# Kernel optimization log

Measured on AMD Instinct MI355X. Metric: run time of the kernel, lower is better.

Reference implementation:

```python
import jax, jax.numpy as jnp
import numpy as np

PROJ = 8192     # projDim
THRESH = 1e-8   # numerical-stability epsilon for signed sqrt
L2_EPS = 1e-12  # eps of torch F.normalize


def setup_inputs() -> dict:
    key = jax.random.key(0)
    k1, k2, k3, k4, k5 = jax.random.split(key, 5)
    B, C, H, W = 16, 512, 14, 14
    x = jax.random.normal(k1, (B, C, H, W), dtype=jnp.float32)
    h1 = jax.random.randint(k2, (C,), 0, PROJ, dtype=jnp.int32)
    h2 = jax.random.randint(k3, (C,), 0, PROJ, dtype=jnp.int32)
    s1 = (2 * jax.random.randint(k4, (C,), 0, 2) - 1).astype(jnp.float32)
    s2 = (2 * jax.random.randint(k5, (C,), 0, 2) - 1).astype(jnp.float32)
    return {"x": x, "s1": s1, "s2": s2, "h1": h1, "h2": h2}


def reference(x, s1, s2, h1, h2):
    # x: [B, C, H, W]; h*: [C] hash buckets in [0, PROJ); s*: [C] signs (+-1)
    B, C, H, W = x.shape
    x_flat = jnp.transpose(x, (0, 2, 3, 1)).reshape(-1, C)  # [N, C], N = B*H*W

    def count_sketch(s, h):
        # Equivalent to x_flat @ M with M[c, h[c]] = s[c]: scatter-add of
        # sign-weighted channels into PROJ bins.  -> [N, PROJ]
        return jax.ops.segment_sum((x_flat * s).T, h, num_segments=PROJ).T

    fft1 = jnp.fft.fft(count_sketch(s1, h1), axis=-1)
    fft2 = jnp.fft.fft(count_sketch(s2, h2), axis=-1)
    conv = jnp.fft.ifft(fft1 * fft2, axis=-1).real       # [N, PROJ]
    y = conv.reshape(B, H, W, PROJ).sum(axis=(1, 2))      # sum pool -> [B, PROJ]
    y = jnp.sign(y) * jnp.sqrt(jnp.abs(y) + THRESH)       # signed sqrt
    norm = jnp.linalg.norm(y, axis=1, keepdims=True)
    return y / jnp.maximum(norm, L2_EPS)                  # l2 normalize (dim=1)
```

## Files before the change

kernel.cpp:

```cpp
#include <hip/hip_runtime.h>
#include <math.h>

#define PROJ 8192
#define NB   16
#define NC   512
#define HW   196
#define NKC  7
#define LST  40

typedef __attribute__((ext_vector_type(8))) short bf16x8;
typedef __attribute__((ext_vector_type(4))) short short4v;
typedef __attribute__((ext_vector_type(4))) float f32x4;

__device__ __forceinline__ unsigned bf16_rne(float f) {
    unsigned u = __builtin_bit_cast(unsigned, f);
    return (u + 0x7fffu + ((u >> 16) & 1u)) >> 16;
}

__global__ __launch_bounds__(256)
void cbp_gram_mfma(const float* __restrict__ x,
                   const float* __restrict__ s1,
                   const float* __restrict__ s2,
                   const int*   __restrict__ h1,
                   const int*   __restrict__ h2,
                   float* __restrict__ ws) {
    __shared__ float sk[PROJ];
    __shared__ short Ah[128 * LST];
    __shared__ short Al[128 * LST];
    __shared__ short Bh[128 * LST];
    __shared__ short Bl[128 * LST];
    __shared__ int   lh1[128], lh2[128];
    __shared__ float ls1[128], ls2[128];

    const int tid  = threadIdx.x;
    const int blk  = blockIdx.x;
    const int b    = blk >> 4;
    const int I    = (blk >> 2) & 3;
    const int J    = blk & 3;
    const int c1base = I * 128;
    const int c2base = J * 128;

    const int lane = tid & 63;
    const int wave = tid >> 6;
    const int quad = lane >> 4;
    const int l15  = lane & 15;
    const int wr   = (wave >> 1) * 64;
    const int wc   = (wave & 1) * 64;

    for (int i = tid; i < PROJ; i += 256) sk[i] = 0.f;
    if (tid < 128) {
        lh1[tid] = h1[c1base + tid]; ls1[tid] = s1[c1base + tid];
        lh2[tid] = h2[c2base + tid]; ls2[tid] = s2[c2base + tid];
    }

    const float* xa = x + ((size_t)b * NC + c1base) * HW;
    const float* xb = x + ((size_t)b * NC + c2base) * HW;

    f32x4 acc[4][4];
#pragma unroll
    for (int i = 0; i < 4; ++i)
#pragma unroll
        for (int j = 0; j < 4; ++j)
            acc[i][j] = (f32x4){0.f, 0.f, 0.f, 0.f};

    for (int kc = 0; kc < NKC; ++kc) {
        const int k0 = kc * 32;
        __syncthreads();
#pragma unroll
        for (int it = 0; it < 4; ++it) {
            const int s  = tid + 256 * it;
            const int r  = s >> 3;
            const int q  = s & 7;
            const int kk = k0 + 4 * q;
            float4 va = {0.f, 0.f, 0.f, 0.f}, vb = {0.f, 0.f, 0.f, 0.f};
            if (kk + 3 < HW) {
                va = *(const float4*)&xa[r * HW + kk];
                vb = *(const float4*)&xb[r * HW + kk];
            }
            short4v ah, al, bh, bl;
            const float fa[4] = {va.x, va.y, va.z, va.w};
            const float fb[4] = {vb.x, vb.y, vb.z, vb.w};
#pragma unroll
            for (int c = 0; c < 4; ++c) {
                const unsigned ha_ = bf16_rne(fa[c]);
                ah[c] = (short)ha_;
                al[c] = (short)bf16_rne(fa[c] - __builtin_bit_cast(float, ha_ << 16));
                const unsigned hb_ = bf16_rne(fb[c]);
                bh[c] = (short)hb_;
                bl[c] = (short)bf16_rne(fb[c] - __builtin_bit_cast(float, hb_ << 16));
            }
            *(short4v*)&Ah[r * LST + 4 * q] = ah;
            *(short4v*)&Al[r * LST + 4 * q] = al;
            *(short4v*)&Bh[r * LST + 4 * q] = bh;
            *(short4v*)&Bl[r * LST + 4 * q] = bl;
        }
        __syncthreads();

        bf16x8 ahf[4], alf[4], bhf[4], blf[4];
#pragma unroll
        for (int i = 0; i < 4; ++i) {
            const int ra = wr + i * 16 + l15;
            const int rb = wc + i * 16 + l15;
            ahf[i] = *(const bf16x8*)&Ah[ra * LST + quad * 8];
            alf[i] = *(const bf16x8*)&Al[ra * LST + quad * 8];
            bhf[i] = *(const bf16x8*)&Bh[rb * LST + quad * 8];
            blf[i] = *(const bf16x8*)&Bl[rb * LST + quad * 8];
        }
#pragma unroll
        for (int i = 0; i < 4; ++i)
#pragma unroll
            for (int j = 0; j < 4; ++j) {
                acc[i][j] = __builtin_amdgcn_mfma_f32_16x16x32_bf16(ahf[i], bhf[j], acc[i][j], 0, 0, 0);
                acc[i][j] = __builtin_amdgcn_mfma_f32_16x16x32_bf16(ahf[i], blf[j], acc[i][j], 0, 0, 0);
                acc[i][j] = __builtin_amdgcn_mfma_f32_16x16x32_bf16(alf[i], bhf[j], acc[i][j], 0, 0, 0);
            }
    }
    __syncthreads();

#pragma unroll
    for (int i = 0; i < 4; ++i) {
        const int lr0 = wr + i * 16 + quad * 4;
#pragma unroll
        for (int j = 0; j < 4; ++j) {
            const int lc   = wc + j * 16 + l15;
            const int h2v  = lh2[lc];
            const float s2v = ls2[lc];
#pragma unroll
            for (int rg = 0; rg < 4; ++rg) {
                const int lr  = lr0 + rg;
                const int bin = (lh1[lr] + h2v) & (PROJ - 1);
                atomicAdd(&sk[bin], ls1[lr] * s2v * acc[i][j][rg]);
            }
        }
    }
    __syncthreads();

    float4* dst = (float4*)(ws + (size_t)blk * PROJ);
    const float4* src = (const float4*)sk;
    for (int i = tid; i < PROJ / 4; i += 256) dst[i] = src[i];
}

__global__ __launch_bounds__(256)
void cbp_reduce(const float* __restrict__ ws, float* __restrict__ y,
                float* __restrict__ ssqp) {
    const int blk = blockIdx.x;
    const int b   = blk >> 5;
    const int seg = blk & 31;
    const int tid = threadIdx.x;
    const int bin = seg * 256 + tid;

    const float* base = ws + (size_t)b * 16 * PROJ + bin;
    float s = 0.f;
#pragma unroll
    for (int p = 0; p < 16; ++p) s += base[(size_t)p * PROJ];

    const float m = sqrtf(fabsf(s) + 1e-8f);
    const float o = (s > 0.f) ? m : (s < 0.f ? -m : 0.f);
    y[b * PROJ + bin] = o;

    __shared__ float red[256];
    red[tid] = o * o;
    __syncthreads();
#pragma unroll
    for (int st = 128; st >= 1; st >>= 1) {
        if (tid < st) red[tid] += red[tid + st];
        __syncthreads();
    }
    if (tid == 0) ssqp[blk] = red[0];
}

__global__ __launch_bounds__(256)
void cbp_normalize(float* __restrict__ y, const float* __restrict__ ssqp) {
    const int b   = blockIdx.x >> 1;
    const int off = (blockIdx.x & 1) * 4096;
    const int tid = threadIdx.x;
    float ssq = 0.f;
#pragma unroll
    for (int i = 0; i < 32; ++i) ssq += ssqp[b * 32 + i];
    const float inv = 1.0f / fmaxf(sqrtf(ssq), 1e-12f);

    float4* row = (float4*)&y[(size_t)b * PROJ + off];
#pragma unroll
    for (int j = 0; j < 4; ++j) {
        float4 v = row[j * 256 + tid];
        v.x *= inv; v.y *= inv; v.z *= inv; v.w *= inv;
        row[j * 256 + tid] = v;
    }
}

extern "C" void kernel_launch(void* const* d_in, const int* in_sizes, int n_in,
                              void* d_out, int out_size, void* d_ws, size_t ws_size,
                              hipStream_t stream) {
    const float* x  = (const float*)d_in[0];
    const float* s1 = (const float*)d_in[1];
    const float* s2 = (const float*)d_in[2];
    const int*   h1 = (const int*)d_in[3];
    const int*   h2 = (const int*)d_in[4];
    float* y    = (float*)d_out;
    float* ws   = (float*)d_ws;
    float* ssqp = ws + (size_t)256 * PROJ;

    hipLaunchKernelGGL(cbp_gram_mfma, dim3(NB * 16), dim3(256), 0, stream,
                       x, s1, s2, h1, h2, ws);
    hipLaunchKernelGGL(cbp_reduce, dim3(512), dim3(256), 0, stream, ws, y, ssqp);
    hipLaunchKernelGGL(cbp_normalize, dim3(32), dim3(256), 0, stream, y, ssqp);
}
```

Baseline: 111.2 us.

## Double workgroup size, prefetch next K chunk into registers, fold signs into inputs

The Gram MFMA kernel moves to 512-thread workgroups, so each of 8 waves owns a 32x64 sub-tile instead of 64x64. The next K-chunk of x is now loaded from global memory into registers while the current chunk is converted and computed, to hide load latency behind the bf16 split and MFMA work. The hash signs are multiplied into the inputs before the hi/lo bf16 split, which takes the per-element sign multiplies out of the atomic scatter. The block-to-batch mapping is also remapped to interleave batches, and the reduce kernel's workspace indexing is updated to match. In exchange, each thread holds more registers for the prefetch, and per-wave tiles are smaller, which lowers B-fragment reuse per wave.

After: 104.2 us. -6.3%, faster.

```diff
diff --git a/kernel.cpp b/kernel.cpp
--- a/kernel.cpp
+++ b/kernel.cpp
@@ -17,7 +17,7 @@
     return (u + 0x7fffu + ((u >> 16) & 1u)) >> 16;
 }
 
-__global__ __launch_bounds__(256)
+__global__ __launch_bounds__(512, 2)
 void cbp_gram_mfma(const float* __restrict__ x,
                    const float* __restrict__ s1,
                    const float* __restrict__ s2,
@@ -30,13 +30,13 @@
     __shared__ short Bh[128 * LST];
     __shared__ short Bl[128 * LST];
     __shared__ int   lh1[128], lh2[128];
-    __shared__ float ls1[128], ls2[128];
-
-    const int tid  = threadIdx.x;
-    const int blk  = blockIdx.x;
-    const int b    = blk >> 4;
-    const int I    = (blk >> 2) & 3;
-    const int J    = blk & 3;
+    __shared__ float lsA[128], lsB[128];
+
+    const int tid = threadIdx.x;
+    const int blk = blockIdx.x;
+    const int b    = 2 * (blk & 7) + (blk >> 7);
+    const int tile = (blk >> 3) & 15;
+    const int I = tile >> 2, J = tile & 3;
     const int c1base = I * 128;
     const int c2base = J * 128;
 
@@ -44,42 +44,48 @@
     const int wave = tid >> 6;
     const int quad = lane >> 4;
     const int l15  = lane & 15;
-    const int wr   = (wave >> 1) * 64;
+    const int wr   = (wave >> 1) * 32;
     const int wc   = (wave & 1) * 64;
 
-    for (int i = tid; i < PROJ; i += 256) sk[i] = 0.f;
+    for (int i = tid; i < PROJ; i += 512) sk[i] = 0.f;
     if (tid < 128) {
-        lh1[tid] = h1[c1base + tid]; ls1[tid] = s1[c1base + tid];
-        lh2[tid] = h2[c2base + tid]; ls2[tid] = s2[c2base + tid];
+        lh1[tid] = h1[c1base + tid];  lsA[tid] = s1[c1base + tid];
+        lh2[tid] = h2[c2base + tid];  lsB[tid] = s2[c2base + tid];
     }
 
     const float* xa = x + ((size_t)b * NC + c1base) * HW;
     const float* xb = x + ((size_t)b * NC + c2base) * HW;
 
-    f32x4 acc[4][4];
-#pragma unroll
-    for (int i = 0; i < 4; ++i)
-#pragma unroll
-        for (int j = 0; j < 4; ++j)
-            acc[i][j] = (f32x4){0.f, 0.f, 0.f, 0.f};
+    f32x4 acc[2][4];
+#pragma unroll
+    for (int i = 0; i < 2; ++i)
+#pragma unroll
+        for (int j = 0; j < 4; ++j) acc[i][j] = (f32x4){0.f, 0.f, 0.f, 0.f};
+
+    const int sr0 = tid >> 3;
+    const int sq  = tid & 7;
+
+    float4 pa[2], pb[2];
+    {
+        const int kk = 4 * sq;
+        const bool ok = (kk + 3 < HW);
+#pragma unroll
+        for (int h = 0; h < 2; ++h) {
+            const int r = sr0 + 64 * h;
+            pa[h] = ok ? *(const float4*)&xa[r * HW + kk] : (float4){0.f,0.f,0.f,0.f};
+            pb[h] = ok ? *(const float4*)&xb[r * HW + kk] : (float4){0.f,0.f,0.f,0.f};
+        }
+    }
 
     for (int kc = 0; kc < NKC; ++kc) {
-        const int k0 = kc * 32;
         __syncthreads();
 #pragma unroll
-        for (int it = 0; it < 4; ++it) {
-            const int s  = tid + 256 * it;
-            const int r  = s >> 3;
-            const int q  = s & 7;
-            const int kk = k0 + 4 * q;
-            float4 va = {0.f, 0.f, 0.f, 0.f}, vb = {0.f, 0.f, 0.f, 0.f};
-            if (kk + 3 < HW) {
-                va = *(const float4*)&xa[r * HW + kk];
-                vb = *(const float4*)&xb[r * HW + kk];
-            }
+        for (int h = 0; h < 2; ++h) {
+            const int r = sr0 + 64 * h;
+            const float sA = lsA[r], sB = lsB[r];
+            const float fa[4] = {pa[h].x*sA, pa[h].y*sA, pa[h].z*sA, pa[h].w*sA};
+            const float fb[4] = {pb[h].x*sB, pb[h].y*sB, pb[h].z*sB, pb[h].w*sB};
             short4v ah, al, bh, bl;
-            const float fa[4] = {va.x, va.y, va.z, va.w};
-            const float fb[4] = {vb.x, vb.y, vb.z, vb.w};
 #pragma unroll
             for (int c = 0; c < 4; ++c) {
                 const unsigned ha_ = bf16_rne(fa[c]);
@@ -89,25 +95,38 @@
                 bh[c] = (short)hb_;
                 bl[c] = (short)bf16_rne(fb[c] - __builtin_bit_cast(float, hb_ << 16));
             }
-            *(short4v*)&Ah[r * LST + 4 * q] = ah;
-            *(short4v*)&Al[r * LST + 4 * q] = al;
-            *(short4v*)&Bh[r * LST + 4 * q] = bh;
-            *(short4v*)&Bl[r * LST + 4 * q] = bl;
+            *(short4v*)&Ah[r * LST + 4 * sq] = ah;
+            *(short4v*)&Al[r * LST + 4 * sq] = al;
+            *(short4v*)&Bh[r * LST + 4 * sq] = bh;
+            *(short4v*)&Bl[r * LST + 4 * sq] = bl;
+        }
+        if (kc + 1 < NKC) {
+            const int kk = (kc + 1) * 32 + 4 * sq;
+            const bool ok = (kk + 3 < HW);
+#pragma unroll
+            for (int h = 0; h < 2; ++h) {
+                const int r = sr0 + 64 * h;
+                pa[h] = ok ? *(const float4*)&xa[r * HW + kk] : (float4){0.f,0.f,0.f,0.f};
+                pb[h] = ok ? *(const float4*)&xb[r * HW + kk] : (float4){0.f,0.f,0.f,0.f};
+            }
         }
         __syncthreads();
 
-        bf16x8 ahf[4], alf[4], bhf[4], blf[4];
-#pragma unroll
-        for (int i = 0; i < 4; ++i) {
+        bf16x8 ahf[2], alf[2], bhf[4], blf[4];
+#pragma unroll
+        for (int i = 0; i < 2; ++i) {
             const int ra = wr + i * 16 + l15;
-            const int rb = wc + i * 16 + l15;
             ahf[i] = *(const bf16x8*)&Ah[ra * LST + quad * 8];
             alf[i] = *(const bf16x8*)&Al[ra * LST + quad * 8];
-            bhf[i] = *(const bf16x8*)&Bh[rb * LST + quad * 8];
-            blf[i] = *(const bf16x8*)&Bl[rb * LST + quad * 8];
-        }
-#pragma unroll
-        for (int i = 0; i < 4; ++i)
+        }
+#pragma unroll
+        for (int j = 0; j < 4; ++j) {
+            const int rb = wc + j * 16 + l15;
+            bhf[j] = *(const bf16x8*)&Bh[rb * LST + quad * 8];
+            blf[j] = *(const bf16x8*)&Bl[rb * LST + quad * 8];
+        }
+#pragma unroll
+        for (int i = 0; i < 2; ++i)
 #pragma unroll
             for (int j = 0; j < 4; ++j) {
                 acc[i][j] = __builtin_amdgcn_mfma_f32_16x16x32_bf16(ahf[i], bhf[j], acc[i][j], 0, 0, 0);
@@ -118,18 +137,15 @@
     __syncthreads();
 
 #pragma unroll
-    for (int i = 0; i < 4; ++i) {
+    for (int i = 0; i < 2; ++i) {
         const int lr0 = wr + i * 16 + quad * 4;
 #pragma unroll
         for (int j = 0; j < 4; ++j) {
-            const int lc   = wc + j * 16 + l15;
-            const int h2v  = lh2[lc];
-            const float s2v = ls2[lc];
+            const int h2v = lh2[wc + j * 16 + l15];
 #pragma unroll
             for (int rg = 0; rg < 4; ++rg) {
-                const int lr  = lr0 + rg;
-                const int bin = (lh1[lr] + h2v) & (PROJ - 1);
-                atomicAdd(&sk[bin], ls1[lr] * s2v * acc[i][j][rg]);
+                const int bin = (lh1[lr0 + rg] + h2v) & (PROJ - 1);
+                atomicAdd(&sk[bin], acc[i][j][rg]);
             }
         }
     }
@@ -137,7 +153,7 @@
 
     float4* dst = (float4*)(ws + (size_t)blk * PROJ);
     const float4* src = (const float4*)sk;
-    for (int i = tid; i < PROJ / 4; i += 256) dst[i] = src[i];
+    for (int i = tid; i < PROJ / 4; i += 512) dst[i] = src[i];
 }
 
 __global__ __launch_bounds__(256)
@@ -149,10 +165,11 @@
     const int tid = threadIdx.x;
     const int bin = seg * 256 + tid;
 
-    const float* base = ws + (size_t)b * 16 * PROJ + bin;
+    const int pbase = ((b & 1) << 7) | (b >> 1);
     float s = 0.f;
 #pragma unroll
-    for (int p = 0; p < 16; ++p) s += base[(size_t)p * PROJ];
+    for (int t = 0; t < 16; ++t)
+        s += ws[(size_t)(pbase | (t << 3)) * PROJ + bin];
 
     const float m = sqrtf(fabsf(s) + 1e-8f);
     const float o = (s > 0.f) ? m : (s < 0.f ? -m : 0.f);
@@ -200,7 +217,7 @@
     float* ws   = (float*)d_ws;
     float* ssqp = ws + (size_t)256 * PROJ;
 
-    hipLaunchKernelGGL(cbp_gram_mfma, dim3(NB * 16), dim3(256), 0, stream,
+    hipLaunchKernelGGL(cbp_gram_mfma, dim3(256), dim3(512), 0, stream,
                        x, s1, s2, h1, h2, ws);
     hipLaunchKernelGGL(cbp_reduce, dim3(512), dim3(256), 0, stream, ws, y, ssqp);
     hipLaunchKernelGGL(cbp_normalize, dim3(32), dim3(256), 0, stream, y, ssqp);
```

## Exploit Gram symmetry, pre-split bf16 in prep kernel, load fragments from global

Applied to the files above, without the earlier changes.

Adds a prep kernel that splits x once into padded bf16 hi/lo arrays, so the gram kernel no longer converts from fp32 or stages tiles through shared memory. It reads MFMA fragments straight from global with register double-buffering. The Gram matrix is tiled into 64x64 blocks and only upper-triangular tiles are computed, with each off-diagonal product scattered to both sketch bins. Blocks are mapped across XCDs by batch, and the reduce and normalize kernels are reindexed to match. The cost is an extra launch, extra global traffic for the bf16 copies, more partial buffers to reduce, and doubled atomics on off-diagonal tiles.

Result: slower. 120.1 us (+8.0%).

```diff
diff --git a/kernel.cpp b/kernel.cpp
--- a/kernel.cpp
+++ b/kernel.cpp
@@ -5,8 +5,9 @@
 #define NB   16
 #define NC   512
 #define HW   196
-#define NKC  7
-#define LST  40
+#define KP   224
+#define NROW (NB * NC)
+#define XELE ((size_t)NROW * KP)
 
 typedef __attribute__((ext_vector_type(8))) short bf16x8;
 typedef __attribute__((ext_vector_type(4))) short short4v;
@@ -18,141 +19,143 @@
 }
 
 __global__ __launch_bounds__(256)
-void cbp_gram_mfma(const float* __restrict__ x,
-                   const float* __restrict__ s1,
-                   const float* __restrict__ s2,
-                   const int*   __restrict__ h1,
-                   const int*   __restrict__ h2,
-                   float* __restrict__ ws) {
+void cbp_prep(const float* __restrict__ x,
+              short* __restrict__ xh, short* __restrict__ xl) {
+    const int id  = blockIdx.x * 256 + threadIdx.x;
+    const int q   = id % 56;
+    const int row = id / 56;
+    float4 v = {0.f, 0.f, 0.f, 0.f};
+    if (q < 49) v = *(const float4*)&x[(size_t)row * HW + 4 * q];
+    const float f[4] = {v.x, v.y, v.z, v.w};
+    short4v h, l;
+#pragma unroll
+    for (int c = 0; c < 4; ++c) {
+        const unsigned hb = bf16_rne(f[c]);
+        h[c] = (short)hb;
+        l[c] = (short)bf16_rne(f[c] - __builtin_bit_cast(float, hb << 16));
+    }
+    *(short4v*)&xh[(size_t)row * KP + 4 * q] = h;
+    *(short4v*)&xl[(size_t)row * KP + 4 * q] = l;
+}
+
+#define LOADFRAGS(buf, kc)                                             \
+    {                                                                  \
+        _Pragma("unroll")                                              \
+        for (int i = 0; i < 2; ++i) {                                  \
+            ah[buf][i] = *(const bf16x8*)&pAh[i * 3584 + (kc) * 32];   \
+            al[buf][i] = *(const bf16x8*)&pAl[i * 3584 + (kc) * 32];   \
+            bh[buf][i] = *(const bf16x8*)&pBh[i * 3584 + (kc) * 32];   \
+            bl[buf][i] = *(const bf16x8*)&pBl[i * 3584 + (kc) * 32];   \
+        }                                                              \
+    }
+
+__global__ __launch_bounds__(256, 4)
+void cbp_gram(const short* __restrict__ xh, const short* __restrict__ xl,
+              const float* __restrict__ s1, const float* __restrict__ s2,
+              const int*   __restrict__ h1, const int*   __restrict__ h2,
+              float* __restrict__ partials) {
     __shared__ float sk[PROJ];
-    __shared__ short Ah[128 * LST];
-    __shared__ short Al[128 * LST];
-    __shared__ short Bh[128 * LST];
-    __shared__ short Bl[128 * LST];
-    __shared__ int   lh1[128], lh2[128];
-    __shared__ float ls1[128], ls2[128];
-
-    const int tid  = threadIdx.x;
-    const int blk  = blockIdx.x;
-    const int b    = blk >> 4;
-    const int I    = (blk >> 2) & 3;
-    const int J    = blk & 3;
-    const int c1base = I * 128;
-    const int c2base = J * 128;
-
-    const int lane = tid & 63;
-    const int wave = tid >> 6;
-    const int quad = lane >> 4;
-    const int l15  = lane & 15;
-    const int wr   = (wave >> 1) * 64;
-    const int wc   = (wave & 1) * 64;
+    __shared__ int   rh1[64], rh2[64], ch1[64], ch2[64];
+    __shared__ float rs1[64], rs2[64], cs1[64], cs2[64];
+
+    const int tid = threadIdx.x;
+    const int blk = blockIdx.x;
+    const int xcd = blk & 7;
+    const int idx = blk >> 3;
+    const int hi  = (idx >= 36) ? 1 : 0;
+    const int b   = 2 * xcd + hi;
+    int I = 0, uu = idx - 36 * hi;
+    while (uu >= 8 - I) { uu -= 8 - I; ++I; }
+    const int J = I + uu;
+    const int c1base = I * 64, c2base = J * 64;
 
     for (int i = tid; i < PROJ; i += 256) sk[i] = 0.f;
-    if (tid < 128) {
-        lh1[tid] = h1[c1base + tid]; ls1[tid] = s1[c1base + tid];
-        lh2[tid] = h2[c2base + tid]; ls2[tid] = s2[c2base + tid];
-    }
-
-    const float* xa = x + ((size_t)b * NC + c1base) * HW;
-    const float* xb = x + ((size_t)b * NC + c2base) * HW;
-
-    f32x4 acc[4][4];
-#pragma unroll
-    for (int i = 0; i < 4; ++i)
-#pragma unroll
-        for (int j = 0; j < 4; ++j)
-            acc[i][j] = (f32x4){0.f, 0.f, 0.f, 0.f};
-
-    for (int kc = 0; kc < NKC; ++kc) {
-        const int k0 = kc * 32;
-        __syncthreads();
-#pragma unroll
-        for (int it = 0; it < 4; ++it) {
-            const int s  = tid + 256 * it;
-            const int r  = s >> 3;
-            const int q  = s & 7;
-            const int kk = k0 + 4 * q;
-            float4 va = {0.f, 0.f, 0.f, 0.f}, vb = {0.f, 0.f, 0.f, 0.f};
-            if (kk + 3 < HW) {
-                va = *(const float4*)&xa[r * HW + kk];
-                vb = *(const float4*)&xb[r * HW + kk];
+    if (tid < 64) {
+        rh1[tid] = h1[c1base + tid]; rh2[tid] = h2[c1base + tid];
+        rs1[tid] = s1[c1base + tid]; rs2[tid] = s2[c1base + tid];
+    } else if (tid < 128) {
+        const int t = tid - 64;
+        ch1[t] = h1[c2base + t]; ch2[t] = h2[c2base + t];
+        cs1[t] = s1[c2base + t]; cs2[t] = s2[c2base + t];
+    }
+    __syncthreads();
+
+    const int lane = tid & 63, wave = tid >> 6;
+    const int quad = lane >> 4, l15 = lane & 15;
+    const int wr = (wave >> 1) * 32, wc = (wave & 1) * 32;
+
+    const size_t rowA = ((size_t)b * NC + c1base + wr + l15) * KP + quad * 8;
+    const size_t rowB = ((size_t)b * NC + c2base + wc + l15) * KP + quad * 8;
+    const short* pAh = xh + rowA;  const short* pAl = xl + rowA;
+    const short* pBh = xh + rowB;  const short* pBl = xl + rowB;
+
+    f32x4 acc[2][2];
+#pragma unroll
+    for (int i = 0; i < 2; ++i)
+#pragma unroll
+        for (int j = 0; j < 2; ++j) acc[i][j] = (f32x4){0.f, 0.f, 0.f, 0.f};
+
+    bf16x8 ah[2][2], al[2][2], bh[2][2], bl[2][2];
+    LOADFRAGS(0, 0)
+#pragma unroll
+    for (int kc = 0; kc < 7; ++kc) {
+        const int cur = kc & 1;
+        if (kc < 6) LOADFRAGS(cur ^ 1, kc + 1)
+#pragma unroll
+        for (int i = 0; i < 2; ++i)
+#pragma unroll
+            for (int j = 0; j < 2; ++j) {
+                acc[i][j] = __builtin_amdgcn_mfma_f32_16x16x32_bf16(ah[cur][i], bh[cur][j], acc[i][j], 0, 0, 0);
+                acc[i][j] = __builtin_amdgcn_mfma_f32_16x16x32_bf16(ah[cur][i], bl[cur][j], acc[i][j], 0, 0, 0);
+                acc[i][j] = __builtin_amdgcn_mfma_f32_16x16x32_bf16(al[cur][i], bh[cur][j], acc[i][j], 0, 0, 0);
             }
-            short4v ah, al, bh, bl;
-            const float fa[4] = {va.x, va.y, va.z, va.w};
-            const float fb[4] = {vb.x, vb.y, vb.z, vb.w};
-#pragma unroll
-            for (int c = 0; c < 4; ++c) {
-                const unsigned ha_ = bf16_rne(fa[c]);
-                ah[c] = (short)ha_;
-                al[c] = (short)bf16_rne(fa[c] - __builtin_bit_cast(float, ha_ << 16));
-                const unsigned hb_ = bf16_rne(fb[c]);
-                bh[c] = (short)hb_;
-                bl[c] = (short)bf16_rne(fb[c] - __builtin_bit_cast(float, hb_ << 16));
-            }
-            *(short4v*)&Ah[r * LST + 4 * q] = ah;
-            *(short4v*)&Al[r * LST + 4 * q] = al;
-            *(short4v*)&Bh[r * LST + 4 * q] = bh;
-            *(short4v*)&Bl[r * LST + 4 * q] = bl;
-        }
-        __syncthreads();
-
-        bf16x8 ahf[4], alf[4], bhf[4], blf[4];
-#pragma unroll
-        for (int i = 0; i < 4; ++i) {
-            const int ra = wr + i * 16 + l15;
-            const int rb = wc + i * 16 + l15;
-            ahf[i] = *(const bf16x8*)&Ah[ra * LST + quad * 8];
-            alf[i] = *(const bf16x8*)&Al[ra * LST + quad * 8];
-            bhf[i] = *(const bf16x8*)&Bh[rb * LST + quad * 8];
-            blf[i] = *(const bf16x8*)&Bl[rb * LST + quad * 8];
-        }
-#pragma unroll
-        for (int i = 0; i < 4; ++i)
-#pragma unroll
-            for (int j = 0; j < 4; ++j) {
-                acc[i][j] = __builtin_amdgcn_mfma_f32_16x16x32_bf16(ahf[i], bhf[j], acc[i][j], 0, 0, 0);
-                acc[i][j] = __builtin_amdgcn_mfma_f32_16x16x32_bf16(ahf[i], blf[j], acc[i][j], 0, 0, 0);
-                acc[i][j] = __builtin_amdgcn_mfma_f32_16x16x32_bf16(alf[i], bhf[j], acc[i][j], 0, 0, 0);
-            }
-    }
-    __syncthreads();
-
-#pragma unroll
-    for (int i = 0; i < 4; ++i) {
-        const int lr0 = wr + i * 16 + quad * 4;
-#pragma unroll
-        for (int j = 0; j < 4; ++j) {
-            const int lc   = wc + j * 16 + l15;
-            const int h2v  = lh2[lc];
-            const float s2v = ls2[lc];
+    }
+
+    const bool offd = (I != J);
+#pragma unroll
+    for (int i = 0; i < 2; ++i) {
+        const int r0 = wr + i * 16 + quad * 4;
+#pragma unroll
+        for (int j = 0; j < 2; ++j) {
+            const int c = wc + j * 16 + l15;
+            const int ch2v = ch2[c], ch1v = ch1[c];
+            const float cs2v = cs2[c], cs1v = cs1[c];
 #pragma unroll
             for (int rg = 0; rg < 4; ++rg) {
-                const int lr  = lr0 + rg;
-                const int bin = (lh1[lr] + h2v) & (PROJ - 1);
-                atomicAdd(&sk[bin], ls1[lr] * s2v * acc[i][j][rg]);
+                const int r = r0 + rg;
+                const float g = acc[i][j][rg];
+                atomicAdd(&sk[(rh1[r] + ch2v) & (PROJ - 1)], rs1[r] * cs2v * g);
+                if (offd)
+                    atomicAdd(&sk[(ch1v + rh2[r]) & (PROJ - 1)], cs1v * rs2[r] * g);
             }
         }
     }
     __syncthreads();
 
-    float4* dst = (float4*)(ws + (size_t)blk * PROJ);
+    float4* dst = (float4*)(partials + (size_t)blk * PROJ);
     const float4* src = (const float4*)sk;
     for (int i = tid; i < PROJ / 4; i += 256) dst[i] = src[i];
 }
 
 __global__ __launch_bounds__(256)
-void cbp_reduce(const float* __restrict__ ws, float* __restrict__ y,
+void cbp_reduce(const float* __restrict__ partials, float* __restrict__ y,
                 float* __restrict__ ssqp) {
     const int blk = blockIdx.x;
-    const int b   = blk >> 5;
-    const int seg = blk & 31;
+    const int xcd = blk & 7;
+    const int k   = blk >> 3;
+    const int hi  = k >> 5;
+    const int seg = k & 31;
+    const int b   = 2 * xcd + hi;
     const int tid = threadIdx.x;
     const int bin = seg * 256 + tid;
 
-    const float* base = ws + (size_t)b * 16 * PROJ + bin;
     float s = 0.f;
 #pragma unroll
-    for (int p = 0; p < 16; ++p) s += base[(size_t)p * PROJ];
+    for (int u = 0; u < 36; ++u) {
+        int u2 = u + seg; if (u2 >= 36) u2 -= 36;
+        const int pb = ((hi * 36 + u2) << 3) | xcd;
+        s += partials[(size_t)pb * PROJ + bin];
+    }
 
     const float m = sqrtf(fabsf(s) + 1e-8f);
     const float o = (s > 0.f) ? m : (s < 0.f ? -m : 0.f);
@@ -176,7 +179,8 @@
     const int tid = threadIdx.x;
     float ssq = 0.f;
 #pragma unroll
-    for (int i = 0; i < 32; ++i) ssq += ssqp[b * 32 + i];
+    for (int seg = 0; seg < 32; ++seg)
+        ssq += ssqp[(((b & 1) * 32 + seg) << 3) | (b >> 1)];
     const float inv = 1.0f / fmaxf(sqrtf(ssq), 1e-12f);
 
     float4* row = (float4*)&y[(size_t)b * PROJ + off];
@@ -196,12 +200,17 @@
     const float* s2 = (const float*)d_in[2];
     const int*   h1 = (const int*)d_in[3];
     const int*   h2 = (const int*)d_in[4];
-    float* y    = (float*)d_out;
-    float* ws   = (float*)d_ws;
-    float* ssqp = ws + (size_t)256 * PROJ;
-
-    hipLaunchKernelGGL(cbp_gram_mfma, dim3(NB * 16), dim3(256), 0, stream,
-                       x, s1, s2, h1, h2, ws);
-    hipLaunchKernelGGL(cbp_reduce, dim3(512), dim3(256), 0, stream, ws, y, ssqp);
+    float* y = (float*)d_out;
+
+    short* xh = (short*)d_ws;
+    short* xl = xh + XELE;
+    float* partials = (float*)(xl + XELE);
+    float* ssqp = partials + (size_t)576 * PROJ;
+
+    hipLaunchKernelGGL(cbp_prep, dim3(1792), dim3(256), 0, stream, x, xh, xl);
+    hipLaunchKernelGGL(cbp_gram, dim3(576), dim3(256), 0, stream,
+                       xh, xl, s1, s2, h1, h2, partials);
+    hipLaunchKernelGGL(cbp_reduce, dim3(512), dim3(256), 0, stream,
+                       partials, y, ssqp);
     hipLaunchKernelGGL(cbp_normalize, dim3(32), dim3(256), 0, stream, y, ssqp);
 }
```
